# Performance work log

Hardware: AMD Instinct MI355X
Metric: run time of the kernel (lower is better)

Reference implementation:

```python
import jax, jax.numpy as jnp
import numpy as np

EPSILON = 0.01  # from init_kwargs

def setup_inputs() -> dict:
    key = jax.random.key(0)
    k1, k2, k3, k4 = jax.random.split(key, 4)
    N, E, D = 100000, 3200000, 4
    x = jax.random.normal(k1, (N, D), dtype=jnp.float32)
    edge_index = jax.random.randint(k2, (2, E), 0, N, dtype=jnp.int32)
    boo_values = jax.random.normal(k3, (E, D, D), dtype=jnp.float32)
    mask = jnp.ones((N, 1), dtype=jnp.float32)
    diag = jax.random.uniform(k4, (N, D), dtype=jnp.float32)
    return {"x": x, "edge_index": edge_index, "boo_values": boo_values,
            "mask": mask, "diag": diag}

def reference(x, edge_index, boo_values, mask, diag):
    # y = eps*diag*x + A @ (diag * (A^T @ x)), A blocked-sparse with
    # per-edge blocks A_{row,col} = boo_values[e] in R^{DxD}.
    N = x.shape[0]
    row, col = edge_index[0], edge_index[1]
    # spmv_t (A^T x): gather x at row i, message A_ij^T x_i, scatter-add to col j
    msg_t = jnp.einsum('eji,ej->ei', boo_values, x[row])  # [E, D]
    AT_x = jax.ops.segment_sum(msg_t, col, num_segments=N) * mask  # [N, D]
    eps_x = EPSILON * x
    AT_x = AT_x * diag
    eps_x = eps_x * diag
    # spmv (A v): gather v at col j, message A_ij v_j, scatter-add to row i
    msg = jnp.einsum('eij,ej->ei', boo_values, AT_x[col])  # [E, D]
    A_AT_x = jax.ops.segment_sum(msg, row, num_segments=N) * mask  # [N, D]
    return eps_x + A_AT_x
```

## Files before the change

### kernel.cpp

```cpp
#include <hip/hip_runtime.h>

#define EPSILON 0.01f

#define BLK    256
#define SLICE  1024
#define SLOG   10
#define PCH    20
#define BCH    4096
#define MAXS   128


__global__ void init_cursors(int* cur1, int* cur2, int S, int cap) {
    int t = threadIdx.x;
    if (t < S) { cur1[t] = t * cap; cur2[t] = t * cap; }
}

__global__ void __launch_bounds__(BLK) bin_kernel(
    const int* __restrict__ row, const int* __restrict__ col,
    int2* __restrict__ bins1, int2* __restrict__ bins2,
    int* __restrict__ cur1, int* __restrict__ cur2,
    long long E, int S)
{
    __shared__ int2 st[BCH];
    __shared__ unsigned char ss[BCH];
    __shared__ int hist[MAXS], rnk[MAXS], sbase[MAXS], gbase[MAXS];
    const int t = threadIdx.x;

    long long start = (long long)blockIdx.x * BCH;
    long long endl  = start + BCH; if (endl > E) endl = E;
    const int cnt = (int)(endl - start);

    for (int side = 0; side < 2; ++side) {
        const int* __restrict__ key = side ? row : col;
        const int* __restrict__ oth = side ? col : row;
        int2* __restrict__ bins = side ? bins2 : bins1;
        int*  __restrict__ cur  = side ? cur2  : cur1;

        if (t < MAXS) { hist[t] = 0; rnk[t] = 0; }
        __syncthreads();

        for (int i0 = t * 4; i0 < cnt; i0 += BLK * 4) {
            if (i0 + 4 <= cnt) {
                int4 k = *reinterpret_cast<const int4*>(key + start + i0);
                atomicAdd(&hist[k.x >> SLOG], 1);
                atomicAdd(&hist[k.y >> SLOG], 1);
                atomicAdd(&hist[k.z >> SLOG], 1);
                atomicAdd(&hist[k.w >> SLOG], 1);
            } else {
                for (int i = i0; i < cnt; ++i)
                    atomicAdd(&hist[key[start + i] >> SLOG], 1);
            }
        }
        __syncthreads();

        if (t == 0) {
            int run = 0;
            for (int s2 = 0; s2 < S; ++s2) { sbase[s2] = run; run += hist[s2]; }
        }
        if (t < S) gbase[t] = atomicAdd(&cur[t], hist[t]);
        __syncthreads();

        for (int i0 = t * 4; i0 < cnt; i0 += BLK * 4) {
            if (i0 + 4 <= cnt) {
                int4 k = *reinterpret_cast<const int4*>(key + start + i0);
                int4 o = *reinterpret_cast<const int4*>(oth + start + i0);
                int kk[4] = {k.x, k.y, k.z, k.w};
                int oo[4] = {o.x, o.y, o.z, o.w};
                #pragma unroll
                for (int u = 0; u < 4; ++u) {
                    int s2 = kk[u] >> SLOG;
                    int slot = sbase[s2] + atomicAdd(&rnk[s2], 1);
                    st[slot] = make_int2((int)(start + i0 + u),
                                         ((kk[u] & (SLICE - 1)) << 17) | oo[u]);
                    ss[slot] = (unsigned char)s2;
                }
            } else {
                for (int i = i0; i < cnt; ++i) {
                    int kv = key[start + i], ov = oth[start + i];
                    int s2 = kv >> SLOG;
                    int slot = sbase[s2] + atomicAdd(&rnk[s2], 1);
                    st[slot] = make_int2((int)(start + i),
                                         ((kv & (SLICE - 1)) << 17) | ov);
                    ss[slot] = (unsigned char)s2;
                }
            }
        }
        __syncthreads();

        for (int i = t; i < cnt; i += BLK) {
            int s2 = ss[i];
            bins[(size_t)gbase[s2] + (i - sbase[s2])] = st[i];
        }
        __syncthreads();
    }
}

template<int PASS, int STAGED>
__global__ void __launch_bounds__(BLK) pass_kernel(
    const float4* __restrict__ boo,
    const int2*   __restrict__ bins,
    const int*    __restrict__ cur,
    const float4* __restrict__ src,
    const float*  __restrict__ mask,
    float*        __restrict__ dst,
    int N, int cap, int P)
{
    __shared__ float acc[SLICE * 4];

    const int s    = blockIdx.x / P;
    const int p    = blockIdx.x - s * P;
    const int base = s << SLOG;
    const int lim  = min(SLICE, N - base);

    for (int i = threadIdx.x; i < SLICE * 4; i += BLK) acc[i] = 0.0f;
    __syncthreads();

    const int cnt = cur[s] - s * cap;
    const int lo  = (int)((long long)cnt * p / P);
    const int hi  = (int)((long long)cnt * (p + 1) / P);
    const int2* __restrict__ bin = bins + (size_t)s * cap;

    const int j  = (int)(threadIdx.x & 3);
    const int g0 = (int)(threadIdx.x >> 2);

    auto process = [&](int2 rec, float4 b) {
        float4 v = src[rec.y & 0x1FFFF];
        int loc = ((unsigned)rec.y) >> 17;
        float val;
        if (PASS == 2) {
            val = b.x * v.x + b.y * v.y + b.z * v.z + b.w * v.w;
        } else {
            float xj = (j == 0) ? v.x : (j == 1) ? v.y : (j == 2) ? v.z : v.w;
            float4 q;
            q.x = b.x * xj; q.y = b.y * xj; q.z = b.z * xj; q.w = b.w * xj;
            q.x += __shfl_xor(q.x, 1); q.y += __shfl_xor(q.y, 1);
            q.z += __shfl_xor(q.z, 1); q.w += __shfl_xor(q.w, 1);
            q.x += __shfl_xor(q.x, 2); q.y += __shfl_xor(q.y, 2);
            q.z += __shfl_xor(q.z, 2); q.w += __shfl_xor(q.w, 2);
            val = (j == 0) ? q.x : (j == 1) ? q.y : (j == 2) ? q.z : q.w;
        }
        atomicAdd(&acc[loc * 4 + j], val);
    };

    int i = lo + g0;
    for (; i + 64 < hi; i += 128) {
        int2 ra = bin[i];
        int2 rb = bin[i + 64];
        float4 ba = boo[(long long)ra.x * 4 + j];
        float4 bb = boo[(long long)rb.x * 4 + j];
        process(ra, ba);
        process(rb, bb);
    }
    if (i < hi) {
        int2 ra = bin[i];
        float4 ba = boo[(long long)ra.x * 4 + j];
        process(ra, ba);
    }
    __syncthreads();

    if (STAGED) {
        float* stg = dst + (size_t)blockIdx.x * (SLICE * 4);
        for (int f = threadIdx.x; f < lim * 4; f += BLK) stg[f] = acc[f];
    } else if (PASS == 1) {
        for (int f = threadIdx.x; f < lim * 4; f += BLK)
            unsafeAtomicAdd(dst + ((long long)base * 4 + f), acc[f]);
    } else {
        for (int f = threadIdx.x; f < lim * 4; f += BLK) {
            float mv = mask[base + (f >> 2)];
            unsafeAtomicAdd(dst + ((long long)base * 4 + f), acc[f] * mv);
        }
    }
}

__global__ void __launch_bounds__(BLK) mid_staged_kernel(
    const float4* __restrict__ stage,
    const float4* __restrict__ d4,
    const float*  __restrict__ mask,
    float4* __restrict__ v4,
    int N, int P)
{
    int n = blockIdx.x * BLK + threadIdx.x;
    if (n >= N) return;
    int s = n >> SLOG, local = n & (SLICE - 1);
    const float4* t = stage + ((size_t)s * P) * SLICE + local;
    float4 a = make_float4(0.f, 0.f, 0.f, 0.f);
    for (int p = 0; p < P; ++p) {
        float4 u = t[(size_t)p * SLICE];
        a.x += u.x; a.y += u.y; a.z += u.z; a.w += u.w;
    }
    float4 dv = d4[n];
    float  m  = mask[n];
    a.x *= dv.x * m; a.y *= dv.y * m; a.z *= dv.z * m; a.w *= dv.w * m;
    v4[n] = a;
}

__global__ void __launch_bounds__(BLK) fin_staged_kernel(
    const float4* __restrict__ stage,
    const float4* __restrict__ x4,
    const float4* __restrict__ d4,
    const float*  __restrict__ mask,
    float4* __restrict__ out4,
    int N, int P)
{
    int n = blockIdx.x * BLK + threadIdx.x;
    if (n >= N) return;
    int s = n >> SLOG, local = n & (SLICE - 1);
    const float4* t = stage + ((size_t)s * P) * SLICE + local;
    float4 a = make_float4(0.f, 0.f, 0.f, 0.f);
    for (int p = 0; p < P; ++p) {
        float4 u = t[(size_t)p * SLICE];
        a.x += u.x; a.y += u.y; a.z += u.z; a.w += u.w;
    }
    float4 xv = x4[n];
    float4 dv = d4[n];
    float  m  = mask[n];
    float4 o;
    o.x = EPSILON * xv.x * dv.x + a.x * m;
    o.y = EPSILON * xv.y * dv.y + a.y * m;
    o.z = EPSILON * xv.z * dv.z + a.z * m;
    o.w = EPSILON * xv.w * dv.w + a.w * m;
    out4[n] = o;
}

__global__ void __launch_bounds__(BLK) mid_atomic_kernel(
    const float4* __restrict__ x4,
    const float4* __restrict__ d4,
    const float*  __restrict__ mask,
    float4* __restrict__ atx,
    float4* __restrict__ out4,
    int N)
{
    int n = blockIdx.x * BLK + threadIdx.x;
    if (n >= N) return;
    float4 a  = atx[n];
    float4 dv = d4[n];
    float  m  = mask[n];
    a.x *= dv.x * m; a.y *= dv.y * m; a.z *= dv.z * m; a.w *= dv.w * m;
    atx[n] = a;
    float4 xv = x4[n];
    float4 o;
    o.x = EPSILON * xv.x * dv.x; o.y = EPSILON * xv.y * dv.y;
    o.z = EPSILON * xv.z * dv.z; o.w = EPSILON * xv.w * dv.w;
    out4[n] = o;
}

__global__ void __launch_bounds__(256) spmvt_kernel(
    const float4* __restrict__ boo, const int* __restrict__ row,
    const int* __restrict__ col, const float* __restrict__ x,
    float* __restrict__ ATx, long long E)
{
    long long t = (long long)blockIdx.x * blockDim.x + threadIdx.x;
    long long e = t >> 2;
    int j = (int)(t & 3);
    if (e >= E) return;
    float4 b = boo[e * 4 + j];
    int r = row[e];
    float xj = x[r * 4 + j];
    float4 p;
    p.x = b.x * xj; p.y = b.y * xj; p.z = b.z * xj; p.w = b.w * xj;
    p.x += __shfl_xor(p.x, 1); p.y += __shfl_xor(p.y, 1);
    p.z += __shfl_xor(p.z, 1); p.w += __shfl_xor(p.w, 1);
    p.x += __shfl_xor(p.x, 2); p.y += __shfl_xor(p.y, 2);
    p.z += __shfl_xor(p.z, 2); p.w += __shfl_xor(p.w, 2);
    float v = (j == 0) ? p.x : (j == 1) ? p.y : (j == 2) ? p.z : p.w;
    int c = col[e];
    unsafeAtomicAdd(&ATx[c * 4 + j], v);
}

__global__ void __launch_bounds__(256) spmv_kernel(
    const float4* __restrict__ boo, const int* __restrict__ row,
    const int* __restrict__ col, const float* __restrict__ vv,
    const float* __restrict__ mask, float* __restrict__ out, long long E)
{
    long long t = (long long)blockIdx.x * blockDim.x + threadIdx.x;
    long long e = t >> 2;
    int i = (int)(t & 3);
    if (e >= E) return;
    float4 b = boo[e * 4 + i];
    int c = col[e];
    const float4* v4 = (const float4*)vv;
    float4 v = v4[c];
    float mi = b.x * v.x + b.y * v.y + b.z * v.z + b.w * v.w;
    int r = row[e];
    float mr = mask[r];
    unsafeAtomicAdd(&out[r * 4 + i], mi * mr);
}

extern "C" void kernel_launch(void* const* d_in, const int* in_sizes, int n_in,
                              void* d_out, int out_size, void* d_ws, size_t ws_size,
                              hipStream_t stream) {
    const float* x    = (const float*)d_in[0];
    const int*   ei   = (const int*)d_in[1];
    const float* boo  = (const float*)d_in[2];
    const float* mask = (const float*)d_in[3];
    const float* diag = (const float*)d_in[4];
    float* out = (float*)d_out;

    int N = in_sizes[0] / 4;
    long long E = in_sizes[1] / 2;
    const int* row = ei;
    const int* col = ei + E;

    int S = (N + SLICE - 1) >> SLOG;
    int cap = (int)((E + S - 1) / S);
    cap += cap * 3 / 10;
    cap = (cap + 255) & ~255;

    size_t o_v   = 0;
    size_t o_cur = ((size_t)N * 16 + 255) & ~(size_t)255;
    size_t o_b1  = o_cur + 2048;
    size_t szb   = (size_t)S * cap * 8;
    size_t o_b2  = o_b1 + szb;
    size_t o_st  = o_b2 + szb;
    size_t szst  = (size_t)S * PCH * SLICE * 16;

    bool ok   = (S <= MAXS) && (N <= (1 << 17));
    int  tier = (!ok) ? 3 : (ws_size >= o_st + szst) ? 1
                          : (ws_size >= o_st)        ? 2 : 3;

    float* v     = (float*)((char*)d_ws + o_v);
    int*   cur1  = (int*)((char*)d_ws + o_cur);
    int*   cur2  = cur1 + 256;
    int2*  bins1 = (int2*)((char*)d_ws + o_b1);
    int2*  bins2 = (int2*)((char*)d_ws + o_b2);
    float* stage = (float*)((char*)d_ws + o_st);

    const int gNode = (N + BLK - 1) / BLK;
    const int gBin  = (int)((E + BCH - 1) / BCH);
    const int gPass = S * PCH;

    if (tier <= 2) {
        init_cursors<<<1, MAXS, 0, stream>>>(cur1, cur2, S, cap);
        bin_kernel<<<gBin, BLK, 0, stream>>>(row, col, bins1, bins2, cur1, cur2, E, S);
        if (tier == 1) {
            pass_kernel<1, 1><<<gPass, BLK, 0, stream>>>(
                (const float4*)boo, bins1, cur1, (const float4*)x, mask, stage, N, cap, PCH);
            mid_staged_kernel<<<gNode, BLK, 0, stream>>>(
                (const float4*)stage, (const float4*)diag, mask, (float4*)v, N, PCH);
            pass_kernel<2, 1><<<gPass, BLK, 0, stream>>>(
                (const float4*)boo, bins2, cur2, (const float4*)v, mask, stage, N, cap, PCH);
            fin_staged_kernel<<<gNode, BLK, 0, stream>>>(
                (const float4*)stage, (const float4*)x, (const float4*)diag, mask,
                (float4*)out, N, PCH);
        } else {
            hipMemsetAsync(v, 0, (size_t)N * 16, stream);
            pass_kernel<1, 0><<<gPass, BLK, 0, stream>>>(
                (const float4*)boo, bins1, cur1, (const float4*)x, mask, v, N, cap, PCH);
            mid_atomic_kernel<<<gNode, BLK, 0, stream>>>(
                (const float4*)x, (const float4*)diag, mask, (float4*)v, (float4*)out, N);
            pass_kernel<2, 0><<<gPass, BLK, 0, stream>>>(
                (const float4*)boo, bins2, cur2, (const float4*)v, mask, out, N, cap, PCH);
        }
    } else {
        hipMemsetAsync(v, 0, (size_t)N * 16, stream);
        long long T = E * 4;
        int gEdge = (int)((T + BLK - 1) / BLK);
        spmvt_kernel<<<gEdge, BLK, 0, stream>>>(
            (const float4*)boo, row, col, x, v, E);
        mid_atomic_kernel<<<gNode, BLK, 0, stream>>>(
            (const float4*)x, (const float4*)diag, mask, (float4*)v, (float4*)out, N);
        spmv_kernel<<<gEdge, BLK, 0, stream>>>(
            (const float4*)boo, row, col, v, mask, out, E);
    }
}
```

Before: 508.6 us.

## Permute edge blocks into slice-sorted order during binning for coalesced pass reads

Adds a binning kernel that, besides sorting edge records by destination slice, also copies each edge's 4x4 block into a slice-contiguous buffer. The pass kernels then read the blocks sequentially instead of gathering them by edge id. Each pass now bins separately and writes 4-byte records, which drops the 8-byte bins. The cost is an extra full read and write of the block array for each pass, plus a larger workspace. The bin slack is also reduced, and the old atomic tier path is removed.

```diff
diff --git a/kernel.cpp b/kernel.cpp
--- a/kernel.cpp
+++ b/kernel.cpp
@@ -10,9 +10,160 @@
 #define MAXS   128
 
 
-__global__ void init_cursors(int* cur1, int* cur2, int S, int cap) {
+__global__ void init_cursors(int* cur, int S, int cap) {
+    int t = threadIdx.x;
+    if (t < S) cur[t] = t * cap;
+}
+
+__global__ void init_cursors2(int* cur1, int* cur2, int S, int cap) {
     int t = threadIdx.x;
     if (t < S) { cur1[t] = t * cap; cur2[t] = t * cap; }
+}
+
+__global__ void __launch_bounds__(BLK) bin_perm_kernel(
+    const int*    __restrict__ key,
+    const int*    __restrict__ oth,
+    const float4* __restrict__ boo,
+    int*          __restrict__ recs,
+    float4*       __restrict__ booP,
+    int*          __restrict__ cur,
+    long long E, int S)
+{
+    __shared__ int2 st[BCH];
+    __shared__ unsigned char ss[BCH];
+    __shared__ int hist[MAXS], rnk[MAXS], sbase[MAXS], gbase[MAXS];
+    const int t = threadIdx.x;
+
+    long long start = (long long)blockIdx.x * BCH;
+    long long endl  = start + BCH; if (endl > E) endl = E;
+    const int cnt = (int)(endl - start);
+
+    if (t < MAXS) { hist[t] = 0; rnk[t] = 0; }
+    __syncthreads();
+
+    for (int i0 = t * 4; i0 < cnt; i0 += BLK * 4) {
+        if (i0 + 4 <= cnt) {
+            int4 k = *reinterpret_cast<const int4*>(key + start + i0);
+            atomicAdd(&hist[k.x >> SLOG], 1);
+            atomicAdd(&hist[k.y >> SLOG], 1);
+            atomicAdd(&hist[k.z >> SLOG], 1);
+            atomicAdd(&hist[k.w >> SLOG], 1);
+        } else {
+            for (int i = i0; i < cnt; ++i)
+                atomicAdd(&hist[key[start + i] >> SLOG], 1);
+        }
+    }
+    __syncthreads();
+
+    if (t == 0) {
+        int run = 0;
+        for (int s2 = 0; s2 < S; ++s2) { sbase[s2] = run; run += hist[s2]; }
+    }
+    if (t < S) gbase[t] = atomicAdd(&cur[t], hist[t]);
+    __syncthreads();
+
+    for (int i0 = t * 4; i0 < cnt; i0 += BLK * 4) {
+        if (i0 + 4 <= cnt) {
+            int4 k = *reinterpret_cast<const int4*>(key + start + i0);
+            int4 o = *reinterpret_cast<const int4*>(oth + start + i0);
+            int kk[4] = {k.x, k.y, k.z, k.w};
+            int oo[4] = {o.x, o.y, o.z, o.w};
+            #pragma unroll
+            for (int u = 0; u < 4; ++u) {
+                int s2 = kk[u] >> SLOG;
+                int slot = sbase[s2] + atomicAdd(&rnk[s2], 1);
+                st[slot] = make_int2((int)(start + i0 + u),
+                                     ((kk[u] & (SLICE - 1)) << 17) | oo[u]);
+                ss[slot] = (unsigned char)s2;
+            }
+        } else {
+            for (int i = i0; i < cnt; ++i) {
+                int kv = key[start + i], ov = oth[start + i];
+                int s2 = kv >> SLOG;
+                int slot = sbase[s2] + atomicAdd(&rnk[s2], 1);
+                st[slot] = make_int2((int)(start + i),
+                                     ((kv & (SLICE - 1)) << 17) | ov);
+                ss[slot] = (unsigned char)s2;
+            }
+        }
+    }
+    __syncthreads();
+
+    for (int i = t; i < cnt; i += BLK) {
+        int s2 = ss[i];
+        recs[(size_t)gbase[s2] + (i - sbase[s2])] = st[i].y;
+    }
+
+    const int j  = t & 3;
+    const int g0 = t >> 2;
+    for (int i = g0; i < cnt; i += 64) {
+        int s2 = ss[i];
+        size_t gp = (size_t)gbase[s2] + (i - sbase[s2]);
+        booP[gp * 4 + j] = boo[(size_t)st[i].x * 4 + j];
+    }
+}
+
+template<int PASS>
+__global__ void __launch_bounds__(BLK) pass_perm_kernel(
+    const float4* __restrict__ booP,
+    const int*    __restrict__ recs,
+    const int*    __restrict__ cur,
+    const float4* __restrict__ src,
+    float*        __restrict__ stage,
+    int N, int cap, int P)
+{
+    __shared__ float acc[SLICE * 4];
+
+    const int s    = blockIdx.x / P;
+    const int p    = blockIdx.x - s * P;
+    const int base = s << SLOG;
+    const int lim  = min(SLICE, N - base);
+
+    for (int i = threadIdx.x; i < SLICE * 4; i += BLK) acc[i] = 0.0f;
+    __syncthreads();
+
+    const int cnt = cur[s] - s * cap;
+    const int lo  = (int)((long long)cnt * p / P);
+    const int hi  = (int)((long long)cnt * (p + 1) / P);
+    const float4* __restrict__ bp = booP + (size_t)s * cap * 4;
+    const int*    __restrict__ rp = recs + (size_t)s * cap;
+
+    const int j  = (int)(threadIdx.x & 3);
+    const int g0 = (int)(threadIdx.x >> 2);
+
+    auto process = [&](int rec, float4 b) {
+        float4 v = src[rec & 0x1FFFF];
+        int loc = ((unsigned)rec) >> 17;
+        float val;
+        if (PASS == 2) {
+            val = b.x * v.x + b.y * v.y + b.z * v.z + b.w * v.w;
+        } else {
+            float xj = (j == 0) ? v.x : (j == 1) ? v.y : (j == 2) ? v.z : v.w;
+            float4 q;
+            q.x = b.x * xj; q.y = b.y * xj; q.z = b.z * xj; q.w = b.w * xj;
+            q.x += __shfl_xor(q.x, 1); q.y += __shfl_xor(q.y, 1);
+            q.z += __shfl_xor(q.z, 1); q.w += __shfl_xor(q.w, 1);
+            q.x += __shfl_xor(q.x, 2); q.y += __shfl_xor(q.y, 2);
+            q.z += __shfl_xor(q.z, 2); q.w += __shfl_xor(q.w, 2);
+            val = (j == 0) ? q.x : (j == 1) ? q.y : (j == 2) ? q.z : q.w;
+        }
+        atomicAdd(&acc[loc * 4 + j], val);
+    };
+
+    int i = lo + g0;
+    for (; i + 64 < hi; i += 128) {
+        int ra = rp[i];
+        int rb = rp[i + 64];
+        float4 ba = bp[(size_t)i * 4 + j];
+        float4 bb = bp[(size_t)(i + 64) * 4 + j];
+        process(ra, ba);
+        process(rb, bb);
+    }
+    if (i < hi) process(rp[i], bp[(size_t)i * 4 + j]);
+    __syncthreads();
+
+    float* stg = stage + (size_t)blockIdx.x * (SLICE * 4);
+    for (int f = threadIdx.x; f < lim * 4; f += BLK) stg[f] = acc[f];
 }
 
 __global__ void __launch_bounds__(BLK) bin_kernel(
@@ -95,14 +246,13 @@
     }
 }
 
-template<int PASS, int STAGED>
+template<int PASS>
 __global__ void __launch_bounds__(BLK) pass_kernel(
     const float4* __restrict__ boo,
     const int2*   __restrict__ bins,
     const int*    __restrict__ cur,
     const float4* __restrict__ src,
-    const float*  __restrict__ mask,
-    float*        __restrict__ dst,
+    float*        __restrict__ stage,
     int N, int cap, int P)
 {
     __shared__ float acc[SLICE * 4];
@@ -153,23 +303,12 @@
     }
     if (i < hi) {
         int2 ra = bin[i];
-        float4 ba = boo[(long long)ra.x * 4 + j];
-        process(ra, ba);
-    }
-    __syncthreads();
-
-    if (STAGED) {
-        float* stg = dst + (size_t)blockIdx.x * (SLICE * 4);
-        for (int f = threadIdx.x; f < lim * 4; f += BLK) stg[f] = acc[f];
-    } else if (PASS == 1) {
-        for (int f = threadIdx.x; f < lim * 4; f += BLK)
-            unsafeAtomicAdd(dst + ((long long)base * 4 + f), acc[f]);
-    } else {
-        for (int f = threadIdx.x; f < lim * 4; f += BLK) {
-            float mv = mask[base + (f >> 2)];
-            unsafeAtomicAdd(dst + ((long long)base * 4 + f), acc[f] * mv);
-        }
-    }
+        process(ra, boo[(long long)ra.x * 4 + j]);
+    }
+    __syncthreads();
+
+    float* stg = stage + (size_t)blockIdx.x * (SLICE * 4);
+    for (int f = threadIdx.x; f < lim * 4; f += BLK) stg[f] = acc[f];
 }
 
 __global__ void __launch_bounds__(BLK) mid_staged_kernel(
@@ -303,54 +442,73 @@
 
     int S = (N + SLICE - 1) >> SLOG;
     int cap = (int)((E + S - 1) / S);
-    cap += cap * 3 / 10;
+    cap += cap * 12 / 100;
     cap = (cap + 255) & ~255;
 
     size_t o_v   = 0;
     size_t o_cur = ((size_t)N * 16 + 255) & ~(size_t)255;
-    size_t o_b1  = o_cur + 2048;
+    size_t o_rec = o_cur + 1024;
+    size_t szrec = (size_t)S * cap * 4;
+    size_t o_bp  = (o_rec + szrec + 255) & ~(size_t)255;
+    size_t szbp  = (size_t)S * cap * 64;
+    size_t o_st1 = o_bp + szbp;
+    size_t szst  = (size_t)S * PCH * SLICE * 16;
+    size_t need1 = o_st1 + szst;
+
+    size_t o_b1  = o_rec;
     size_t szb   = (size_t)S * cap * 8;
     size_t o_b2  = o_b1 + szb;
-    size_t o_st  = o_b2 + szb;
-    size_t szst  = (size_t)S * PCH * SLICE * 16;
-
-    bool ok   = (S <= MAXS) && (N <= (1 << 17));
-    int  tier = (!ok) ? 3 : (ws_size >= o_st + szst) ? 1
-                          : (ws_size >= o_st)        ? 2 : 3;
-
-    float* v     = (float*)((char*)d_ws + o_v);
-    int*   cur1  = (int*)((char*)d_ws + o_cur);
-    int*   cur2  = cur1 + 256;
-    int2*  bins1 = (int2*)((char*)d_ws + o_b1);
-    int2*  bins2 = (int2*)((char*)d_ws + o_b2);
-    float* stage = (float*)((char*)d_ws + o_st);
+    size_t o_st2 = o_b2 + szb;
+    size_t need2 = o_st2 + szst;
+
+    bool ok   = (S <= MAXS) && (N <= (1 << 17)) && ((E & 3) == 0);
+    int  tier = (!ok) ? 3 : (ws_size >= need1) ? 1
+                          : (ws_size >= need2) ? 2 : 3;
+
+    float* v    = (float*)((char*)d_ws + o_v);
+    int*   cur1 = (int*)((char*)d_ws + o_cur);
+    int*   cur2 = cur1 + 128;
 
     const int gNode = (N + BLK - 1) / BLK;
     const int gBin  = (int)((E + BCH - 1) / BCH);
     const int gPass = S * PCH;
 
-    if (tier <= 2) {
-        init_cursors<<<1, MAXS, 0, stream>>>(cur1, cur2, S, cap);
+    if (tier == 1) {
+        int*    recs  = (int*)((char*)d_ws + o_rec);
+        float4* booP  = (float4*)((char*)d_ws + o_bp);
+        float*  stage = (float*)((char*)d_ws + o_st1);
+
+        init_cursors<<<1, MAXS, 0, stream>>>(cur1, S, cap);
+        bin_perm_kernel<<<gBin, BLK, 0, stream>>>(
+            col, row, (const float4*)boo, recs, booP, cur1, E, S);
+        pass_perm_kernel<1><<<gPass, BLK, 0, stream>>>(
+            booP, recs, cur1, (const float4*)x, stage, N, cap, PCH);
+        mid_staged_kernel<<<gNode, BLK, 0, stream>>>(
+            (const float4*)stage, (const float4*)diag, mask, (float4*)v, N, PCH);
+        init_cursors<<<1, MAXS, 0, stream>>>(cur2, S, cap);
+        bin_perm_kernel<<<gBin, BLK, 0, stream>>>(
+            row, col, (const float4*)boo, recs, booP, cur2, E, S);
+        pass_perm_kernel<2><<<gPass, BLK, 0, stream>>>(
+            booP, recs, cur2, (const float4*)v, stage, N, cap, PCH);
+        fin_staged_kernel<<<gNode, BLK, 0, stream>>>(
+            (const float4*)stage, (const float4*)x, (const float4*)diag, mask,
+            (float4*)out, N, PCH);
+    } else if (tier == 2) {
+        int2*  bins1 = (int2*)((char*)d_ws + o_b1);
+        int2*  bins2 = (int2*)((char*)d_ws + o_b2);
+        float* stage = (float*)((char*)d_ws + o_st2);
+
+        init_cursors2<<<1, MAXS, 0, stream>>>(cur1, cur2, S, cap);
         bin_kernel<<<gBin, BLK, 0, stream>>>(row, col, bins1, bins2, cur1, cur2, E, S);
-        if (tier == 1) {
-            pass_kernel<1, 1><<<gPass, BLK, 0, stream>>>(
-                (const float4*)boo, bins1, cur1, (const float4*)x, mask, stage, N, cap, PCH);
-            mid_staged_kernel<<<gNode, BLK, 0, stream>>>(
-                (const float4*)stage, (const float4*)diag, mask, (float4*)v, N, PCH);
-            pass_kernel<2, 1><<<gPass, BLK, 0, stream>>>(
-                (const float4*)boo, bins2, cur2, (const float4*)v, mask, stage, N, cap, PCH);
-            fin_staged_kernel<<<gNode, BLK, 0, stream>>>(
-                (const float4*)stage, (const float4*)x, (const float4*)diag, mask,
-                (float4*)out, N, PCH);
-        } else {
-            hipMemsetAsync(v, 0, (size_t)N * 16, stream);
-            pass_kernel<1, 0><<<gPass, BLK, 0, stream>>>(
-                (const float4*)boo, bins1, cur1, (const float4*)x, mask, v, N, cap, PCH);
-            mid_atomic_kernel<<<gNode, BLK, 0, stream>>>(
-                (const float4*)x, (const float4*)diag, mask, (float4*)v, (float4*)out, N);
-            pass_kernel<2, 0><<<gPass, BLK, 0, stream>>>(
-                (const float4*)boo, bins2, cur2, (const float4*)v, mask, out, N, cap, PCH);
-        }
+        pass_kernel<1><<<gPass, BLK, 0, stream>>>(
+            (const float4*)boo, bins1, cur1, (const float4*)x, stage, N, cap, PCH);
+        mid_staged_kernel<<<gNode, BLK, 0, stream>>>(
+            (const float4*)stage, (const float4*)diag, mask, (float4*)v, N, PCH);
+        pass_kernel<2><<<gPass, BLK, 0, stream>>>(
+            (const float4*)boo, bins2, cur2, (const float4*)v, stage, N, cap, PCH);
+        fin_staged_kernel<<<gNode, BLK, 0, stream>>>(
+            (const float4*)stage, (const float4*)x, (const float4*)diag, mask,
+            (float4*)out, N, PCH);
     } else {
         hipMemsetAsync(v, 0, (size_t)N * 16, stream);
         long long T = E * 4;
```

After: 712.1 us. +40.0%, slower.
